# Performance work log

Hardware: AMD Instinct MI355X
Metric: run time of the kernel (lower is better)

The kernel has to match this reference:

```python
import jax, jax.numpy as jnp
import numpy as np

B = 16      # number of point clouds
N = 4096    # points per cloud (max segment size, static)
D = 3       # xyz


def setup_inputs() -> dict:
    key = jax.random.key(0)
    k1, k2 = jax.random.split(key)
    pred = jax.random.normal(k1, (B * N, D), dtype=jnp.float32)
    target = jax.random.normal(k2, (B * N, D), dtype=jnp.float32)
    # sorted batch assignment with equal-size segments (so N_max is static)
    batch = jnp.repeat(jnp.arange(B, dtype=jnp.int64), N)
    return {"pred": pred, "target": target, "batch": batch}


def _to_dense_batch(x, batch):
    # Faithful to torch_geometric.utils.to_dense_batch: scatter each point into
    # its (cloud, within-cloud-position) slot; padding slots stay zero.
    T = x.shape[0]
    counts = jax.ops.segment_sum(jnp.ones((T,), jnp.int32), batch, num_segments=B)
    starts = jnp.concatenate([jnp.zeros((1,), jnp.int32), jnp.cumsum(counts)[:-1]])
    pos = jnp.arange(T, dtype=jnp.int32) - starts[batch]
    dense = jnp.zeros((B, N, x.shape[1]), x.dtype).at[batch, pos].set(x)
    return dense


def _chamfer(x, y):
    # pytorch3d.loss.chamfer_distance defaults: squared L2, point_reduction="mean",
    # batch_reduction="mean"; no lengths -> padded zeros count as points (as in source).
    x2 = jnp.sum(x * x, axis=-1)                      # [B, N]
    y2 = jnp.sum(y * y, axis=-1)                      # [B, N]
    xy = jnp.einsum("bid,bjd->bij", x, y)             # [B, N, N]
    d2 = x2[:, :, None] + y2[:, None, :] - 2.0 * xy   # [B, N, N] squared dists
    cham_x = jnp.mean(jnp.min(d2, axis=2), axis=1)    # x -> nearest y, mean over points
    cham_y = jnp.mean(jnp.min(d2, axis=1), axis=1)    # y -> nearest x
    return jnp.mean(cham_x + cham_y)                  # batch mean of summed directions


def reference(pred, target, batch):
    dense_x = _to_dense_batch(pred, batch)
    dense_y = _to_dense_batch(target, batch)
    return _chamfer(dense_x, dense_y)
```

## Files before the change

kernel.cpp:

```cpp
#include <hip/hip_runtime.h>


typedef __attribute__((ext_vector_type(8))) short bf16x8;
typedef __attribute__((ext_vector_type(16))) float floatx16;

#define BB 16
#define NN 4096
#define T  256
#define NW 4
#define RS 2
#define XC (NW * RS * 32)
#define YB 512
#define YT 32
#define NT (YB / YT)
#define ONEBF 0x3F80u
#define FINF  0x7f7f7f7fu

__device__ __forceinline__ unsigned int f2bf(float f) {
    unsigned int u = __float_as_uint(f);
    u += 0x7fffu + ((u >> 16) & 1u);
    return u >> 16;
}
__device__ __forceinline__ float bf2f(unsigned int h) {
    return __uint_as_float(h << 16);
}
__device__ __forceinline__ float tree16(const floatx16& d) {
    float t0 = fminf(fminf(d[0], d[1]), d[2]);
    float t1 = fminf(fminf(d[3], d[4]), d[5]);
    float t2 = fminf(fminf(d[6], d[7]), d[8]);
    float t3 = fminf(fminf(d[9], d[10]), d[11]);
    float t4 = fminf(fminf(d[12], d[13]), d[14]);
    float u0 = fminf(fminf(t0, t1), t2);
    float u1 = fminf(fminf(t3, t4), d[15]);
    return fminf(u0, u1);
}

__global__ __launch_bounds__(T, 2) void chamfer_mfma(
    const float* __restrict__ pred,
    const float* __restrict__ target,
    unsigned int* __restrict__ pmin)
{
    __shared__ uint4 ldsy[2][YB];
    __shared__ unsigned int colp[NW * YB];

    const int b     = blockIdx.y;
    const int xbase = blockIdx.x * XC;
    const int ybase = blockIdx.z * YB;
    const float* prd = pred   + (size_t)b * NN * 3;
    const float* tgt = target + (size_t)b * NN * 3;
    const int tid  = threadIdx.x;
    const int lane = tid & 63, w = tid >> 6;
    const int kg   = lane >> 5, m = lane & 31;

    for (int yl = tid; yl < YB; yl += T) {
        const float* yp = tgt + (size_t)(ybase + yl) * 3;
        float y0 = yp[0], y1 = yp[1], y2 = yp[2];
        unsigned int h0 = f2bf(y0), h1 = f2bf(y1), h2 = f2bf(y2);
        unsigned int H0 = f2bf(-2.f * bf2f(h0));
        unsigned int H1 = f2bf(-2.f * bf2f(h1));
        unsigned int H2 = f2bf(-2.f * bf2f(h2));
        unsigned int L0 = f2bf(-2.f * (y0 - bf2f(h0)));
        unsigned int L1 = f2bf(-2.f * (y1 - bf2f(h1)));
        unsigned int L2 = f2bf(-2.f * (y2 - bf2f(h2)));
        float ysq = fmaf(y0, y0, fmaf(y1, y1, y2 * y2));
        unsigned int sh = f2bf(ysq);
        unsigned int sl = f2bf(ysq - bf2f(sh));
        ldsy[0][yl] = make_uint4(H0 | (H1 << 16), H2 | (H0 << 16),
                                 H1 | (H2 << 16), L0 | (L1 << 16));
        ldsy[1][yl] = make_uint4(L2 | (ONEBF << 16), ONEBF | (sh << 16),
                                 sl, 0u);
    }
    for (int i = tid; i < NW * YB; i += T) colp[i] = FINF;

    unsigned int av[RS][4];
#pragma unroll
    for (int s = 0; s < RS; ++s) {
        int xi = xbase + w * (RS * 32) + s * 32 + m;
        const float* xp = prd + (size_t)xi * 3;
        float x0 = xp[0], x1 = xp[1], x2 = xp[2];
        unsigned int h0 = f2bf(x0), h1 = f2bf(x1), h2 = f2bf(x2);
        unsigned int L0 = f2bf(x0 - bf2f(h0));
        unsigned int L1 = f2bf(x1 - bf2f(h1));
        unsigned int L2 = f2bf(x2 - bf2f(h2));
        float xsq = fmaf(x0, x0, fmaf(x1, x1, x2 * x2));
        unsigned int sh = f2bf(xsq);
        unsigned int sl = f2bf(xsq - bf2f(sh));
        av[s][0] = kg ? (h2 | (sh << 16))    : (h0 | (h1 << 16));
        av[s][1] = kg ? (sl | (ONEBF << 16)) : (h2 | (L0 << 16));
        av[s][2] = kg ? ONEBF                : (L1 | (L2 << 16));
        av[s][3] = kg ? 0u                   : (h0 | (h1 << 16));
    }
    __syncthreads();

    floatx16 acc[RS];
#pragma unroll
    for (int s = 0; s < RS; ++s)
#pragma unroll
        for (int r = 0; r < 16; ++r) acc[s][r] = 3.402823466e38f;
    floatx16 zacc;
#pragma unroll
    for (int r = 0; r < 16; ++r) zacc[r] = 0.f;

    union U { uint4 q; bf16x8 v; };
    uint4 bc0 = ldsy[kg][m];
    uint4 bc1 = ldsy[kg][YT + m];
    for (int t = 0; t < NT; t += 2) {
        int tn = (t + 2 < NT) ? t + 2 : 0;
        uint4 bn0 = ldsy[kg][tn * YT + m];
        uint4 bn1 = ldsy[kg][(tn + 1) * YT + m];
        U bu0; bu0.q = bc0;
        U bu1; bu1.q = bc1;
        float cp0 = 3.402823466e38f, cp1 = 3.402823466e38f;
#pragma unroll
        for (int s = 0; s < RS; ++s) {
            U au; au.q = make_uint4(av[s][0], av[s][1], av[s][2], av[s][3]);
            floatx16 d0 = __builtin_amdgcn_mfma_f32_32x32x16_bf16(
                au.v, bu0.v, zacc, 0, 0, 0);
            floatx16 d1 = __builtin_amdgcn_mfma_f32_32x32x16_bf16(
                au.v, bu1.v, zacc, 0, 0, 0);
#pragma unroll
            for (int r = 0; r < 16; ++r)
                acc[s][r] = fminf(fminf(acc[s][r], d0[r]), d1[r]);
            cp0 = fminf(cp0, tree16(d0));
            cp1 = fminf(cp1, tree16(d1));
        }
        cp0 = fminf(cp0, __shfl_xor(cp0, 32, 64));
        cp1 = fminf(cp1, __shfl_xor(cp1, 32, 64));
        if (kg == 0) {
            colp[w * YB + t * YT + m]       = __float_as_uint(fmaxf(cp0, 0.f));
            colp[w * YB + (t + 1) * YT + m] = __float_as_uint(fmaxf(cp1, 0.f));
        }
        bc0 = bn0; bc1 = bn1;
    }

#pragma unroll
    for (int s = 0; s < RS; ++s) {
#pragma unroll
        for (int r = 0; r < 16; ++r) {
            float v = acc[s][r];
            v = fminf(v, __shfl_xor(v, 1, 64));
            v = fminf(v, __shfl_xor(v, 2, 64));
            v = fminf(v, __shfl_xor(v, 4, 64));
            v = fminf(v, __shfl_xor(v, 8, 64));
            v = fminf(v, __shfl_xor(v, 16, 64));
            if (m == 0) {
                int row = (r & 3) + 8 * (r >> 2) + 4 * kg;
                int xi  = xbase + w * (RS * 32) + s * 32 + row;
                atomicMin(&pmin[b * NN + xi], __float_as_uint(fmaxf(v, 0.f)));
            }
        }
    }

    __syncthreads();
    for (int yl = tid; yl < YB; yl += T) {
        unsigned int v = min(min(colp[yl], colp[YB + yl]),
                             min(colp[2 * YB + yl], colp[3 * YB + yl]));
        atomicMin(&pmin[BB * NN + b * NN + ybase + yl], v);
    }
}

#define TOTX (2 * BB * NN)

__global__ __launch_bounds__(256) void chamfer_reduce(
    const float* __restrict__ pmin, float* __restrict__ out)
{
    float s = 0.f;
    for (int i = blockIdx.x * 256 + threadIdx.x; i < TOTX; i += gridDim.x * 256)
        s += pmin[i];
#pragma unroll
    for (int off = 32; off > 0; off >>= 1)
        s += __shfl_down(s, off, 64);
    __shared__ float wsum[4];
    if ((threadIdx.x & 63) == 0) wsum[threadIdx.x >> 6] = s;
    __syncthreads();
    if (threadIdx.x == 0) {
        float t = wsum[0] + wsum[1] + wsum[2] + wsum[3];
        atomicAdd(out, t * (1.0f / (BB * NN)));
    }
}

extern "C" void kernel_launch(void* const* d_in, const int* in_sizes, int n_in,
                              void* d_out, int out_size, void* d_ws, size_t ws_size,
                              hipStream_t stream) {
    const float* pred   = (const float*)d_in[0];
    const float* target = (const float*)d_in[1];
    float* out = (float*)d_out;
    unsigned int* pmin = (unsigned int*)d_ws;

    hipMemsetAsync(pmin, 0x7f, (size_t)TOTX * sizeof(unsigned int), stream);
    hipMemsetAsync(out, 0, sizeof(float), stream);

    dim3 grid(NN / XC, BB, NN / YB);
    chamfer_mfma<<<grid, T, 0, stream>>>(pred, target, pmin);
    chamfer_reduce<<<128, 256, 0, stream>>>((const float*)pmin, out);
}
```

Baseline: 97.96 us.

## Replace global atomicMin partial minima with per-tile partial buffers reduced in second kernel

Instead of atomicMin into a memset-initialized global min array, each tile writes its row and column partial minima to a dedicated slot in workspace, and a new reduce kernel takes the min across tiles before summing. This removes the large memset and the global atomic contention, and drops the LDS initialization of column partials. In exchange it writes more partial data (one value per tile pair) and the reduce kernel reads more with strided accesses.

Measured after the change: 94.97 us. 3.0% less time.

```diff
diff --git a/kernel.cpp b/kernel.cpp
--- a/kernel.cpp
+++ b/kernel.cpp
@@ -13,8 +13,9 @@
 #define YB 512
 #define YT 32
 #define NT (YB / YT)
+#define NXB (NN / XC)
+#define NYB (NN / YB)
 #define ONEBF 0x3F80u
-#define FINF  0x7f7f7f7fu
 
 __device__ __forceinline__ unsigned int f2bf(float f) {
     unsigned int u = __float_as_uint(f);
@@ -38,14 +39,17 @@
 __global__ __launch_bounds__(T, 2) void chamfer_mfma(
     const float* __restrict__ pred,
     const float* __restrict__ target,
-    unsigned int* __restrict__ pmin)
+    float* __restrict__ rowp,
+    float* __restrict__ colf)
 {
     __shared__ uint4 ldsy[2][YB];
-    __shared__ unsigned int colp[NW * YB];
-
+    __shared__ float colp[NW * YB];
+
+    const int xb    = blockIdx.x;
     const int b     = blockIdx.y;
-    const int xbase = blockIdx.x * XC;
-    const int ybase = blockIdx.z * YB;
+    const int yb    = blockIdx.z;
+    const int xbase = xb * XC;
+    const int ybase = yb * YB;
     const float* prd = pred   + (size_t)b * NN * 3;
     const float* tgt = target + (size_t)b * NN * 3;
     const int tid  = threadIdx.x;
@@ -70,7 +74,6 @@
         ldsy[1][yl] = make_uint4(L2 | (ONEBF << 16), ONEBF | (sh << 16),
                                  sl, 0u);
     }
-    for (int i = tid; i < NW * YB; i += T) colp[i] = FINF;
 
     unsigned int av[RS][4];
 #pragma unroll
@@ -127,12 +130,13 @@
         cp0 = fminf(cp0, __shfl_xor(cp0, 32, 64));
         cp1 = fminf(cp1, __shfl_xor(cp1, 32, 64));
         if (kg == 0) {
-            colp[w * YB + t * YT + m]       = __float_as_uint(fmaxf(cp0, 0.f));
-            colp[w * YB + (t + 1) * YT + m] = __float_as_uint(fmaxf(cp1, 0.f));
+            colp[w * YB + t * YT + m]       = cp0;
+            colp[w * YB + (t + 1) * YT + m] = cp1;
         }
         bc0 = bn0; bc1 = bn1;
     }
 
+    float* rowbase = rowp + ((size_t)(b * NXB + xb) * NYB + yb) * XC;
 #pragma unroll
     for (int s = 0; s < RS; ++s) {
 #pragma unroll
@@ -145,28 +149,41 @@
             v = fminf(v, __shfl_xor(v, 16, 64));
             if (m == 0) {
                 int row = (r & 3) + 8 * (r >> 2) + 4 * kg;
-                int xi  = xbase + w * (RS * 32) + s * 32 + row;
-                atomicMin(&pmin[b * NN + xi], __float_as_uint(fmaxf(v, 0.f)));
+                rowbase[w * (RS * 32) + s * 32 + row] = v;
             }
         }
     }
 
     __syncthreads();
+    float* colbase = colf + ((size_t)(b * NYB + yb) * NXB + xb) * YB;
     for (int yl = tid; yl < YB; yl += T) {
-        unsigned int v = min(min(colp[yl], colp[YB + yl]),
-                             min(colp[2 * YB + yl], colp[3 * YB + yl]));
-        atomicMin(&pmin[BB * NN + b * NN + ybase + yl], v);
-    }
-}
-
-#define TOTX (2 * BB * NN)
-
-__global__ __launch_bounds__(256) void chamfer_reduce(
-    const float* __restrict__ pmin, float* __restrict__ out)
+        float v = fminf(fminf(colp[yl], colp[YB + yl]),
+                        fminf(colp[2 * YB + yl], colp[3 * YB + yl]));
+        colbase[yl] = v;
+    }
+}
+
+__global__ __launch_bounds__(256) void chamfer_reduce2(
+    const float* __restrict__ rowp, const float* __restrict__ colf,
+    float* __restrict__ out)
 {
-    float s = 0.f;
-    for (int i = blockIdx.x * 256 + threadIdx.x; i < TOTX; i += gridDim.x * 256)
-        s += pmin[i];
+    int e = blockIdx.x * 256 + threadIdx.x;
+    float v = 3.402823466e38f;
+    if (e < BB * NN) {
+        int b = e >> 12, xi = e & (NN - 1);
+        int xb = xi >> 8, li = xi & (XC - 1);
+        const float* p = rowp + ((size_t)(b * NXB + xb) * NYB) * XC + li;
+#pragma unroll
+        for (int yb = 0; yb < NYB; ++yb) v = fminf(v, p[yb * XC]);
+    } else {
+        int f = e - BB * NN;
+        int b = f >> 12, y = f & (NN - 1);
+        int yb = y >> 9, yl = y & (YB - 1);
+        const float* p = colf + ((size_t)(b * NYB + yb) * NXB) * YB + yl;
+#pragma unroll
+        for (int xb = 0; xb < NXB; ++xb) v = fminf(v, p[xb * YB]);
+    }
+    float s = fmaxf(v, 0.f);
 #pragma unroll
     for (int off = 32; off > 0; off >>= 1)
         s += __shfl_down(s, off, 64);
@@ -184,13 +201,12 @@
                               hipStream_t stream) {
     const float* pred   = (const float*)d_in[0];
     const float* target = (const float*)d_in[1];
-    float* out = (float*)d_out;
-    unsigned int* pmin = (unsigned int*)d_ws;
-
-    hipMemsetAsync(pmin, 0x7f, (size_t)TOTX * sizeof(unsigned int), stream);
+    float* out  = (float*)d_out;
+    float* rowp = (float*)d_ws;
+    float* colf = rowp + (size_t)BB * NXB * NYB * XC;
+
     hipMemsetAsync(out, 0, sizeof(float), stream);
-
-    dim3 grid(NN / XC, BB, NN / YB);
-    chamfer_mfma<<<grid, T, 0, stream>>>(pred, target, pmin);
-    chamfer_reduce<<<128, 256, 0, stream>>>((const float*)pmin, out);
-}
+    dim3 grid(NXB, BB, NYB);
+    chamfer_mfma<<<grid, T, 0, stream>>>(pred, target, rowp, colf);
+    chamfer_reduce2<<<512, 256, 0, stream>>>(rowp, colf, out);
+}
```
